# Kernel tuning notes

Measured on AMD Instinct MI355X. Metric: run time of the kernel, lower is better.

## Reference

```python
import jax, jax.numpy as jnp
import numpy as np
from math import factorial, pi, sqrt

N_ATOMS = 4096
N_PAIRS = 49152
F = 16           # num_tensordense_features
NUM_RADIAL = 16  # basis num=16
NUM_SPECIES = 95
EMB_DIM = 32
CUTOFF = 5.0
LMAX = 4         # SelfAttention max_degree=4
NLM = 25
LMAX_B = 2       # basis max_degree=2 (also max_tensordense_degree)
NLM_B = 9

DEG9 = np.repeat(np.arange(3), [1, 3, 5])        # degree index of each lm, l<=2
DEG25 = np.repeat(np.arange(5), [1, 3, 5, 7, 9]) # degree index of each lm, l<=4


def real_sph(u, lmax):
    # real spherical harmonics (m = -l..l ordering, no Condon-Shortley), u: (...,3) unit vectors
    x, y, z = u[..., 0], u[..., 1], u[..., 2]
    phi = jnp.arctan2(y, x)
    ct = jnp.clip(z, -1.0, 1.0)
    st = jnp.sqrt(jnp.clip(1.0 - ct * ct, 0.0, 1.0))
    P = {(0, 0): jnp.ones_like(ct)}
    for m in range(1, lmax + 1):
        P[(m, m)] = -(2 * m - 1) * st * P[(m - 1, m - 1)]
    for m in range(0, lmax):
        P[(m + 1, m)] = (2 * m + 1) * ct * P[(m, m)]
    for m in range(0, lmax + 1):
        for l in range(m + 2, lmax + 1):
            P[(l, m)] = ((2 * l - 1) * ct * P[(l - 1, m)] - (l + m - 1) * P[(l - 2, m)]) / (l - m)
    outs = []
    for l in range(lmax + 1):
        for m in range(-l, l + 1):
            ma = abs(m)
            Nn = sqrt((2 * l + 1) / (4 * pi) * factorial(l - ma) / factorial(l + ma))
            cs = (-1.0) ** ma  # cancel Condon-Shortley in P
            if m == 0:
                Y = Nn * P[(l, 0)]
            elif m > 0:
                Y = sqrt(2.0) * Nn * cs * jnp.cos(m * phi) * P[(l, m)]
            else:
                Y = sqrt(2.0) * Nn * cs * jnp.sin(ma * phi) * P[(l, ma)]
            outs.append(Y)
    return jnp.stack(outs, axis=-1)


def _gaunt():
    # exact real Gaunt (CG-equivalent) coupling coefficients via Gauss-Legendre x uniform-phi quadrature
    nt, nph = 16, 32
    xs, ws = np.polynomial.legendre.leggauss(nt)
    phis = np.arange(nph) * (2 * np.pi / nph)
    ct = np.repeat(xs, nph); ph = np.tile(phis, nt)
    st = np.sqrt(np.clip(1.0 - ct ** 2, 0.0, 1.0))
    u = np.stack([st * np.cos(ph), st * np.sin(ph), ct], -1)
    w = np.repeat(ws, nph) * (2 * np.pi / nph)
    Y = np.asarray(real_sph(jnp.asarray(u, dtype=jnp.float32), LMAX))
    G = np.einsum('gi,gj,gk,g->ijk', Y, Y[:, :NLM_B], Y, w)
    G[np.abs(G) < 1e-6] = 0.0
    return G

_G = _gaunt()
G_ATT = jnp.asarray(_G, dtype=jnp.float32)                      # (25, 9, 25): feat x basis -> feat
G_TD = jnp.asarray(_G[:NLM_B, :, :NLM_B], dtype=jnp.float32)    # (9, 9, 9): TensorDense coupling


def pdense(x, W, deg):
    return jnp.einsum('plf,lfg->plg', x, W[deg])


def couple(xf, Bf, G):
    # equivariant tensor product  out[p,k,f] = sum_ij G[i,j,k] xf[p,i,f] Bf[p,j,f]
    u = jnp.einsum('pif,ijk->pjkf', xf, G)
    return jnp.einsum('pjf,pjkf->pkf', Bf, u)


def setup_inputs() -> dict:
    key = jax.random.key(0)
    ks = jax.random.split(key, 24)
    s = 1.0 / np.sqrt(F)
    inp = dict(
        atomic_numbers=jax.random.randint(ks[0], (N_ATOMS,), 0, NUM_SPECIES),
        neighbour_indices=jnp.stack([
            jax.random.randint(ks[1], (N_PAIRS,), 0, N_ATOMS),
            jax.random.randint(ks[2], (N_PAIRS,), 0, N_ATOMS)], axis=-1),
        neighbour_displacements=jax.random.normal(ks[3], (N_PAIRS, 3), dtype=jnp.float32) * 1.7,
        W_rad=jax.random.normal(ks[4], (NUM_SPECIES, NUM_RADIAL, F), dtype=jnp.float32) / np.sqrt(NUM_RADIAL),
        emb_table=jax.random.normal(ks[5], (NUM_SPECIES, EMB_DIM), dtype=jnp.float32),
        W_emb=jax.random.normal(ks[6], (EMB_DIM, F), dtype=jnp.float32) / np.sqrt(EMB_DIM),
        b_emb=jnp.zeros((F,), jnp.float32),
        td_W1=jax.random.normal(ks[7], (3, F, F), dtype=jnp.float32) * s,
        td_W2=jax.random.normal(ks[8], (3, F, F), dtype=jnp.float32) * s,
        td_W3=jax.random.normal(ks[9], (3, F, F), dtype=jnp.float32) * s,
        Wb1=jax.random.normal(ks[10], (NUM_RADIAL, F), dtype=jnp.float32) / np.sqrt(NUM_RADIAL),
        Wq1=jax.random.normal(ks[11], (5, F, F), dtype=jnp.float32) * s,
        Wk1=jax.random.normal(ks[12], (5, F, F), dtype=jnp.float32) * s,
        Wv1=jax.random.normal(ks[13], (5, F, F), dtype=jnp.float32) * s,
        Wo1=jax.random.normal(ks[14], (5, F, F), dtype=jnp.float32) * s,
        bo1=jnp.zeros((F,), jnp.float32),
        Wb2=jax.random.normal(ks[15], (NUM_RADIAL, F), dtype=jnp.float32) / np.sqrt(NUM_RADIAL),
        Wq2=jax.random.normal(ks[16], (5, F, F), dtype=jnp.float32) * s,
        Wk2=jax.random.normal(ks[17], (5, F, F), dtype=jnp.float32) * s,
        Wv2=jax.random.normal(ks[18], (5, F, F), dtype=jnp.float32) * s,
        Wo2=jax.random.normal(ks[19], (5, F, F), dtype=jnp.float32) * s,
        bo2=jnp.zeros((F,), jnp.float32),
    )
    return inp


def reference(atomic_numbers, neighbour_indices, neighbour_displacements,
              W_rad, emb_table, W_emb, b_emb, td_W1, td_W2, td_W3,
              Wb1, Wq1, Wk1, Wv1, Wo1, bo1, Wb2, Wq2, Wk2, Wv2, Wo2, bo2):
    dst = neighbour_indices[:, 0]   # idx_i
    src = neighbour_indices[:, 1]   # idx_j
    Zj = atomic_numbers[src]
    r = jnp.linalg.norm(neighbour_displacements, axis=-1)
    u = neighbour_displacements / jnp.maximum(r, 1e-9)[:, None]
    sh = real_sph(u, LMAX)          # (P, 25)
    sh_b = sh[:, :NLM_B]            # (P, 9)
    kk = jnp.arange(1, NUM_RADIAL + 1, dtype=jnp.float32)
    rb = jnp.sinc(kk[None, :] * r[:, None] / CUTOFF) * (r < CUTOFF)[:, None]  # sinc basis w/ cutoff
    # species-aware radial basis -> per-pair equivariant features (P, 9, F)
    y0 = jnp.einsum('pk,pkf->pf', rb, W_rad[Zj])
    y = sh_b[:, :, None] * y0[:, None, :]
    # TensorDense: dense -> CG tensor product -> dense (degrees <= 2)
    a = pdense(y, td_W1, DEG9)
    b = pdense(y, td_W2, DEG9)
    u9 = jnp.einsum('pif,ijk->pjkf', a, G_TD)
    tp = jnp.einsum('pjf,pjkf->pkf', b, u9)
    y = pdense(tp, td_W3, DEG9)
    # aggregate per-pair messages to atoms (segment mean), pad degrees to l<=4
    sums = jnp.zeros((N_ATOMS, NLM_B, F), y.dtype).at[dst].add(y)
    cnt = jnp.zeros((N_ATOMS,), y.dtype).at[dst].add(1.0)
    x = sums / jnp.maximum(cnt, 1.0)[:, None, None]
    x = jnp.pad(x, ((0, 0), (0, NLM - NLM_B), (0, 0)))  # (N, 25, F)
    # two segment self-attention layers over neighbour pairs
    for (Wb, Wq, Wk, Wv, Wo, bo) in ((Wb1, Wq1, Wk1, Wv1, Wo1, bo1), (Wb2, Wq2, Wk2, Wv2, Wo2, bo2)):
        Bf = sh_b[:, :, None] * (rb @ Wb)[:, None, :]   # projected pair basis (P, 9, F)
        q = pdense(x, Wq, DEG25)[dst]
        kf = couple(pdense(x, Wk, DEG25)[src], Bf, G_ATT)
        vf = couple(pdense(x, Wv, DEG25)[src], Bf, G_ATT)
        s = jnp.einsum('plf,plf->p', q, kf) / np.sqrt(NLM * F)
        m = jax.lax.stop_gradient(jnp.full((N_ATOMS,), -1e30, s.dtype).at[dst].max(s))
        e = jnp.exp(s - m[dst])
        den = jnp.zeros((N_ATOMS,), s.dtype).at[dst].add(e)
        alpha = e / (den[dst] + 1e-9)
        agg = jnp.zeros((N_ATOMS, NLM, F), x.dtype).at[dst].add(alpha[:, None, None] * vf)
        x = pdense(agg, Wo, DEG25)
        x = x.at[:, 0, :].add(bo)
    # embedding residual connection on the scalar (l=0) channel
    res = emb_table[atomic_numbers] @ W_emb + b_emb
    x = x.at[:, 0, :].add(res)
    return x
```

## Files before the change

### kernel.cpp

```cpp
#include <hip/hip_runtime.h>
#include <hip/hip_bf16.h>

#define NA 4096
#define NP 49152

typedef _Float16 f16;
typedef _Float16 h2 __attribute__((ext_vector_type(2)));
union U4H { uint4 u; f16 h[8]; h2 p[4]; };

__device__ __forceinline__ float fdot2(h2 a, h2 b, float c){
#if __has_builtin(__builtin_amdgcn_fdot2)
  return __builtin_amdgcn_fdot2(a, b, c, false);
#else
  return c + (float)a.x*(float)b.x + (float)a.y*(float)b.y;
#endif
}

constexpr int WS_AOFS9 = 64;
constexpr int WS_ATTW9 = 128;
constexpr int WS_ATTIJ9= WS_ATTW9 + 512;
constexpr int WS_G     = 12800;
constexpr int WS_NATT  = WS_G + 5632;
constexpr int WS_ATTW  = WS_NATT + 8;
constexpr int WS_ATTIJ = WS_ATTW + 1024;
constexpr int WS_TDOFS = WS_ATTIJ + 1024;
constexpr int WS_TDW   = WS_TDOFS + 16;
constexpr int WS_TDIJ  = WS_TDW + 512;
constexpr int WS_AOFS  = WS_TDIJ + 512;
constexpr int WS_SH    = WS_AOFS + 32;
constexpr int WS_RB    = WS_SH + NP*9;
constexpr int WS_S     = WS_RB + NP*16;
constexpr int WS_CCNT  = WS_S + NP;
constexpr int WS_COFF  = WS_CCNT + NA;
constexpr int WS_CCUR  = WS_COFF + NA + 8;
constexpr int WS_CLST  = WS_CCUR + NA;
constexpr int WS_XQ    = WS_CLST + NP;
constexpr int WS_XK    = WS_XQ + NA*400;
constexpr int WS_XV    = WS_XK + NA*400;
constexpr int WS_PVF   = WS_XV + NA*400;
constexpr int WS_WW    = WS_PVF + NP*128;
constexpr int WS_PVFE  = WS_PVF + NP*256;
constexpr int WS_DS    = WS_PVFE;
constexpr long long WS_END = (long long)WS_DS + 2*NP + 16;

__device__ const float  GLX[16] = {
  -0.98940093499164993f, -0.94457502307323258f, -0.86563120238783174f, -0.75540440835500303f,
  -0.61787624440264375f, -0.45801677765722739f, -0.28160355077925891f, -0.09501250983763744f,
   0.09501250983763744f,  0.28160355077925891f,  0.45801677765722739f,  0.61787624440264375f,
   0.75540440835500303f,  0.86563120238783174f,  0.94457502307323258f,  0.98940093499164993f };
__device__ const double GLW[16] = {
  0.02715245941175409, 0.06225352393864789, 0.09515851168249278, 0.12462897125553387,
  0.14959598881657673, 0.16915651939500254, 0.18260341504492359, 0.18945061045506850,
  0.18945061045506850, 0.18260341504492359, 0.16915651939500254, 0.14959598881657673,
  0.12462897125553387, 0.09515851168249278, 0.06225352393864789, 0.02715245941175409 };

#define PI_D 3.14159265358979323846

__device__ __forceinline__ float scrub(float v){
  if(!(v == v)) return 0.f;
  return fminf(fmaxf(v, -1e30f), 1e30f);
}

__device__ void real_sph25(float ct, float phi, float* Y){
  float st = sqrtf(fmaxf(0.f, 1.f - ct*ct));
  float P[5][5];
  P[0][0] = 1.f;
  #pragma unroll
  for(int m=1;m<=4;m++) P[m][m] = -(2.f*m - 1.f)*st*P[m-1][m-1];
  #pragma unroll
  for(int m=0;m<4;m++) P[m+1][m] = (2.f*m + 1.f)*ct*P[m][m];
  #pragma unroll
  for(int m=0;m<=4;m++){
    #pragma unroll
    for(int l=m+2;l<=4;l++)
      P[l][m] = ((2.f*l - 1.f)*ct*P[l-1][m] - (float)(l+m-1)*P[l-2][m]) / (float)(l-m);
  }
  const double fact[9] = {1,1,2,6,24,120,720,5040,40320};
  int idx = 0;
  #pragma unroll
  for(int l=0;l<=4;l++){
    #pragma unroll
    for(int m=-l;m<=l;m++){
      int ma = (m < 0) ? -m : m;
      float Nn = (float)sqrt((2*l+1)/(4.0*PI_D)*fact[l-ma]/fact[l+ma]);
      float cs = (ma & 1) ? -1.f : 1.f;
      float v;
      if(m == 0)      v = Nn * P[l][0];
      else if(m > 0)  v = 1.4142135623730951f * Nn * cs * cosf(ma*phi) * P[l][ma];
      else            v = 1.4142135623730951f * Nn * cs * sinf(ma*phi) * P[l][ma];
      Y[idx++] = v;
    }
  }
}

__global__ __launch_bounds__(256) void k_u1(const float* Wrad, const float* W1,
    const float* W2, const int* nbr, float* ws){
  __shared__ float Ysh[12800];
  int b = blockIdx.x, tid = threadIdx.x;
  if(b < 176){
    for(int pt=tid; pt<512; pt+=256){
      float ct  = GLX[pt >> 5];
      float phi = (float)((pt & 31) * (2.0*PI_D/32.0));
      float Y[25];
      real_sph25(ct, phi, Y);
      #pragma unroll
      for(int i=0;i<25;i++) Ysh[pt*25 + i] = Y[i];
    }
    __syncthreads();
    int idx = b*256 + tid;
    int t = idx >> 3, chunk = idx & 7;
    if(t >= 5625) return;
    int k = t % 25, j = (t/25) % 9, i = t/225;
    double acc = 0.0;
    int g0 = chunk*64;
    #pragma unroll 4
    for(int g=g0; g<g0+64; g++){
      double w = GLW[g >> 5] * (2.0*PI_D/32.0);
      acc += w * (double)Ysh[g*25+i] * (double)Ysh[g*25+j] * (double)Ysh[g*25+k];
    }
    acc += __shfl_xor(acc, 1, 8);
    acc += __shfl_xor(acc, 2, 8);
    acc += __shfl_xor(acc, 4, 8);
    if(chunk == 0){
      if(fabs(acc) < 1e-6) acc = 0.0;
      ws[WS_G + (i*9+j)*25 + k] = (float)acc;
    }
  } else if(b < 271){
    int s = b - 176;
    #pragma unroll
    for(int it=0; it<6; it++){
      int idx = tid + 256*it;
      int w = idx / 768, r = idx % 768;
      int d = r / 256, r2 = r % 256, k = r2 / 16, g = r2 % 16;
      const float* Wsrc = (w == 0) ? W1 : W2;
      float acc = 0.f;
      #pragma unroll
      for(int fp=0; fp<16; fp++)
        acc += Wrad[(s*16+k)*16+fp] * Wsrc[(d*16+fp)*16+g];
      ws[WS_WW + ((size_t)(s*2+w)*16 + g)*48 + d*16 + k] = acc;
    }
  } else {
    int p = (b-271)*256 + tid;
    if(p < NP) atomicAdd((int*)ws + WS_CCNT + nbr[2*p], 1);
  }
}

__global__ __launch_bounds__(1024) void k_scan(float* ws){
  __shared__ int wsum[17];
  int t = threadIdx.x;
  const int* cnt = (const int*)ws + WS_CCNT;
  int v0 = cnt[4*t], v1 = cnt[4*t+1], v2 = cnt[4*t+2], v3 = cnt[4*t+3];
  int s = v0+v1+v2+v3;
  int lane = t & 63, w = t >> 6;
  int x = s;
  #pragma unroll
  for(int o=1;o<64;o<<=1){
    int y = __shfl_up(x, o);
    if(lane >= o) x += y;
  }
  if(lane == 63) wsum[w] = x;
  __syncthreads();
  if(t == 0){
    int run = 0;
    #pragma unroll
    for(int i=0;i<16;i++){ int tmp = wsum[i]; wsum[i] = run; run += tmp; }
    wsum[16] = run;
  }
  __syncthreads();
  int base = wsum[w] + x - s;
  int* offp = (int*)ws + WS_COFF;
  int* cur  = (int*)ws + WS_CCUR;
  offp[4*t]   = base;          cur[4*t]   = base;
  offp[4*t+1] = base+v0;       cur[4*t+1] = base+v0;
  offp[4*t+2] = base+v0+v1;    cur[4*t+2] = base+v0+v1;
  offp[4*t+3] = base+v0+v1+v2; cur[4*t+3] = base+v0+v1+v2;
  if(t == 1023) offp[4096] = wsum[16];
}

__global__ __launch_bounds__(256) void k_u2(const float* disp, const int* nbr, float* ws){
  __shared__ float Gsh[5632];
  __shared__ int cA[25], cT[9], cA9[25], oA[26], oT[10], oA9[26];
  if(blockIdx.x == 0){
    int t = threadIdx.x;
    for(int i=t; i<5625; i+=256) Gsh[i] = ws[WS_G + i];
    __syncthreads();
    const float* G = Gsh;
    if(t < 25){
      int c=0, c9=0;
      for(int i=0;i<25;i++) for(int j=0;j<9;j++) if(G[(i*9+j)*25+t] != 0.f){ c++; if(i<9) c9++; }
      cA[t]=c; cA9[t]=c9;
    }
    if(t < 9){ int c=0; for(int i=0;i<9;i++) for(int j=0;j<9;j++) if(G[(i*9+j)*25+t] != 0.f) c++; cT[t]=c; }
    __syncthreads();
    if(t == 0){
      int s=0; for(int k=0;k<25;k++){ oA[k]=s; s+=cA[k]; } oA[25]=s;
      ((int*)ws)[WS_NATT] = s;
      s=0; for(int k=0;k<25;k++){ oA9[k]=s; s+=cA9[k]; } oA9[25]=s;
      s=0; for(int k=0;k<9;k++){ oT[k]=s; s+=cT[k]; } oT[9]=s;
    }
    __syncthreads();
    float* attw = ws + WS_ATTW;  int* attij = (int*)ws + WS_ATTIJ;
    float* attw9 = ws + WS_ATTW9; int* attij9 = (int*)ws + WS_ATTIJ9;
    int* aofs  = (int*)ws + WS_AOFS;
    int* aofs9 = (int*)ws + WS_AOFS9;
    if(t < 26){ aofs[t] = oA[t] < 1024 ? oA[t] : 1024; aofs9[t] = oA9[t] < 512 ? oA9[t] : 512; }
    if(t < 25){
      int pos = oA[t], pos9 = oA9[t];
      for(int i=0;i<25;i++) for(int j=0;j<9;j++){
        float w = G[(i*9+j)*25+t];
        if(w != 0.f){
          if(pos < 1024){ attw[pos]=w; attij[pos] = i | (j<<5) | (t<<9); pos++; }
          if(i < 9 && pos9 < 512){ attw9[pos9]=w; attij9[pos9] = i | (j<<5) | (t<<9); pos9++; }
        }
      }
    }
    float* tdw = ws + WS_TDW; int* tdij = (int*)ws + WS_TDIJ; int* tdofs = (int*)ws + WS_TDOFS;
    if(t < 9){
      int pos = oT[t];
      for(int i=0;i<9;i++) for(int j=0;j<9;j++){
        float w = G[(i*9+j)*25+t];
        if(w != 0.f && pos < 512){
          int li = (i==0)?0:(i<4)?1:2, lj = (j==0)?0:(j<4)?1:2;
          tdw[pos]=w; tdij[pos] = i | (j<<5) | (li<<10) | (lj<<12); pos++;
        }
      }
      tdofs[t] = oT[t];
      if(t == 0) tdofs[9] = oT[9];
    }
  } else {
    int p = (blockIdx.x-1)*256 + threadIdx.x;
    if(p >= NP) return;
    int d = nbr[2*p], s = nbr[2*p+1];
    int sp = atomicAdd((int*)ws + WS_CCUR + d, 1);
    ((int*)ws)[WS_DS + 2*sp]     = d;
    ((int*)ws)[WS_DS + 2*sp + 1] = s;
    float dx = disp[3*p], dy = disp[3*p+1], dz = disp[3*p+2];
    float r = sqrtf(dx*dx + dy*dy + dz*dz);
    float inv = 1.f / fmaxf(r, 1e-9f);
    float ux = dx*inv, uy = dy*inv, uz = dz*inv;
    float sh[9];
    sh[0] = 0.28209479177387814f;
    sh[1] = 0.4886025119029199f * uy;
    sh[2] = 0.4886025119029199f * uz;
    sh[3] = 0.4886025119029199f * ux;
    sh[4] = 1.0925484305920792f * ux*uy;
    sh[5] = 1.0925484305920792f * uy*uz;
    sh[6] = 0.31539156525252005f * (3.f*uz*uz - 1.f);
    sh[7] = 1.0925484305920792f * ux*uz;
    sh[8] = 0.5462742152960396f * (ux*ux - uy*uy);
    #pragma unroll
    for(int i=0;i<9;i++) ws[WS_SH + sp*9 + i] = scrub(sh[i]);
    float mask = (r < 5.f) ? 1.f : 0.f;
    float rbv[16];
    #pragma unroll
    for(int k=1;k<=16;k++){
      float x  = (float)k * r * 0.2f;
      float px = 3.14159265358979323846f * x;
      float s2 = (px < 1e-6f) ? 1.f : (sinf(px)/px);
      rbv[k-1] = scrub(s2 * mask);
    }
    float4* rb4 = (float4*)(ws + WS_RB + sp*16);
    #pragma unroll
    for(int c=0;c<4;c++) rb4[c] = make_float4(rbv[4*c], rbv[4*c+1], rbv[4*c+2], rbv[4*c+3]);
  }
}

__global__ __launch_bounds__(256) void k_td(const int* aZ, const float* W3, float* ws){
  __shared__ float sh_s[16][9];
  __shared__ float S_s[16][88];
  __shared__ float tp_s[16][9][16];
  int tid = threadIdx.x, pl = tid >> 4, g = tid & 15;
  int sp = blockIdx.x*16 + pl;
  int src = ((const int*)ws)[WS_DS + 2*sp + 1];
  int Zj = aZ[src];
  {
    float4* S4 = (float4*)&S_s[0][0];
    for(int t0=tid; t0<352; t0+=256) S4[t0] = make_float4(0.f,0.f,0.f,0.f);
  }
  if(g < 9) sh_s[pl][g] = ws[WS_SH + sp*9 + g];
  float rb[16];
  {
    const float4* rb4 = (const float4*)(ws + WS_RB + sp*16);
    #pragma unroll
    for(int c=0;c<4;c++){
      float4 r = rb4[c];
      rb[4*c]=r.x; rb[4*c+1]=r.y; rb[4*c+2]=r.z; rb[4*c+3]=r.w;
    }
  }
  float A1[3], A2[3];
  {
    const float4* w1 = (const float4*)(ws + WS_WW + ((size_t)(Zj*2+0)*16+g)*48);
    const float4* w2 = (const float4*)(ws + WS_WW + ((size_t)(Zj*2+1)*16+g)*48);
    #pragma unroll
    for(int d=0; d<3; d++){
      float a1 = 0.f, a2 = 0.f;
      #pragma unroll
      for(int c=0;c<4;c++){
        float4 x1 = w1[d*4+c], x2 = w2[d*4+c];
        a1 += x1.x*rb[4*c] + x1.y*rb[4*c+1] + x1.z*rb[4*c+2] + x1.w*rb[4*c+3];
        a2 += x2.x*rb[4*c] + x2.y*rb[4*c+1] + x2.z*rb[4*c+2] + x2.w*rb[4*c+3];
      }
      A1[d] = a1; A2[d] = a2;
    }
  }
  __syncthreads();
  if(g < 9){
    const float* tdw = ws + WS_TDW;
    const int* tdij  = (const int*)ws + WS_TDIJ;
    const int* tdofs = (const int*)ws + WS_TDOFS;
    int e1 = tdofs[g+1];
    for(int e=tdofs[g]; e<e1; e++){
      float w = tdw[e]; int meta = tdij[e];
      int i = meta & 31, j = (meta>>5) & 15, li = (meta>>10) & 3, lj = (meta>>12) & 3;
      S_s[pl][g*9 + li*3 + lj] += w * sh_s[pl][i] * sh_s[pl][j];
    }
  }
  __syncthreads();
  float AA[9];
  #pragma unroll
  for(int li=0;li<3;li++)
    #pragma unroll
    for(int lj=0;lj<3;lj++) AA[li*3+lj] = A1[li]*A2[lj];
  #pragma unroll
  for(int k=0;k<9;k++){
    float tpv = 0.f;
    #pragma unroll
    for(int c=0;c<9;c++) tpv += S_s[pl][k*9+c] * AA[c];
    tp_s[pl][k][g] = tpv;
  }
  __syncthreads();
  float w3r[48];
  #pragma unroll
  for(int d=0;d<3;d++)
    #pragma unroll
    for(int f2=0;f2<16;f2++) w3r[d*16+f2] = W3[(d*16+f2)*16+g];
  float acc9[9];
  #pragma unroll
  for(int k=0;k<9;k++){
    int d = (k==0)?0:(k<4)?1:2;
    const float4* t4 = (const float4*)&tp_s[pl][k][0];
    float acc = 0.f;
    #pragma unroll
    for(int c=0;c<4;c++){
      float4 t = t4[c];
      acc += t.x*w3r[d*16+4*c] + t.y*w3r[d*16+4*c+1] + t.z*w3r[d*16+4*c+2] + t.w*w3r[d*16+4*c+3];
    }
    acc9[k] = scrub(acc);
  }
  f16* ptd = (f16*)(ws + WS_PVF) + (size_t)sp*256 + g*16;
  U4H u0, u1;
  #pragma unroll
  for(int j=0;j<8;j++) u0.h[j] = (f16)acc9[j];
  u1.h[0] = (f16)acc9[8];
  #pragma unroll
  for(int j=1;j<8;j++) u1.h[j] = (f16)0.f;
  *(uint4*)(ptd)     = u0.u;
  *(uint4*)(ptd + 8) = u1.u;
}

__global__ __launch_bounds__(256) void k_tdq(const float* Wq, const float* Wk,
                                             const float* Wv, float* ws){
  __shared__ float xsh[4][144];
  __shared__ float wq_sh[768], wk_sh[768], wv_sh[768];
  int tid = threadIdx.x, al = tid >> 6, lane = tid & 63;
  int a = blockIdx.x*4 + al;
  for(int t=tid; t<768; t+=256){ wq_sh[t]=Wq[t]; wk_sh[t]=Wk[t]; wv_sh[t]=Wv[t]; }
  const int* coff = (const int*)ws + WS_COFF;
  int off0 = coff[a], n = coff[a+1] - off0;
  const f16* base = (const f16*)(ws + WS_PVF);
  float acc[8] = {0,0,0,0,0,0,0,0};
  if(lane < 32){
    for(int t=0; t<n; t++){
      U4H u; u.u = *(const uint4*)(base + (size_t)(off0+t)*256 + lane*8);
      #pragma unroll
      for(int j=0;j<8;j++) acc[j] += (float)u.h[j];
    }
  }
  float invn = 1.f / fmaxf((float)n, 1.f);
  if(lane < 32){
    int gg = lane >> 1;
    #pragma unroll
    for(int j=0;j<8;j++){
      int k = (lane & 1)*8 + j;
      if(k < 9) xsh[al][k*16 + gg] = scrub(acc[j]*invn);
    }
  }
  __syncthreads();
  int g = lane & 15, q4 = lane >> 4;
  f16* qt = (f16*)(ws + WS_XQ) + (size_t)a*800 + g*32;
  f16* kt = (f16*)(ws + WS_XK) + (size_t)a*800 + g*32;
  f16* vt = (f16*)(ws + WS_XV) + (size_t)a*800 + g*32;
  for(int i=q4; i<16; i+=4){
    if(i < 9){
      int l = (i==0)?0:(i<4)?1:2;
      float q=0.f, k2=0.f, v2=0.f;
      #pragma unroll
      for(int f2=0;f2<16;f2++){
        float xv = xsh[al][i*16+f2];
        q  += xv*wq_sh[(l*16+f2)*16+g];
        k2 += xv*wk_sh[(l*16+f2)*16+g];
        v2 += xv*wv_sh[(l*16+f2)*16+g];
      }
      qt[i] = (f16)q; kt[i] = (f16)k2; vt[i] = (f16)v2;
    } else {
      qt[i] = (f16)0.f; kt[i] = (f16)0.f; vt[i] = (f16)0.f;
    }
  }
}

template<int NI>
__global__ __launch_bounds__(128) void k_att(const float* Wb, float* ws){
  constexpr int MROWH = (NI == 9) ? 16 : 32;
  constexpr int PLSTR = (NI == 9) ? 408 : 840;
  __shared__ __align__(16) f16 Ml[8][PLSTR];
  __shared__ float sh_s[8][9];
  __shared__ float wb_sh[256];
  constexpr int NPAIR = NI/2;
  constexpr int TAIL  = NI-1;
  int tid = threadIdx.x, pl = tid >> 4, g = tid & 15;
  int sp = blockIdx.x*8 + pl;
  {
    uint4 z; z.x=0; z.y=0; z.z=0; z.w=0;
    uint4* Mz = (uint4*)&Ml[0][0];
    for(int t0=tid; t0<PLSTR; t0+=128) Mz[t0] = z;
  }
  for(int t0=tid; t0<256; t0+=128) wb_sh[t0] = Wb[t0];
  if(g < 9) sh_s[pl][g] = ws[WS_SH + sp*9 + g];
  __syncthreads();
  {
    const float* attw = ws + (NI==9 ? WS_ATTW9 : WS_ATTW);
    const int* attij  = (const int*)ws + (NI==9 ? WS_ATTIJ9 : WS_ATTIJ);
    const int* aofs   = (const int*)ws + (NI==9 ? WS_AOFS9 : WS_AOFS);
    for(int kr=g; kr<25; kr+=16){
      f16* Mrow = &Ml[pl][kr*MROWH];
      int e = aofs[kr], e1 = aofs[kr+1];
      if(e < e1){
        int meta = attij[e];
        int curi = meta & 31;
        float cur = 0.f;
        for(; e<e1; e++){
          meta = attij[e];
          int i2 = meta & 31;
          if(i2 != curi){ Mrow[curi] = (f16)cur; cur = 0.f; curi = i2; }
          cur += attw[e] * sh_s[pl][(meta>>5) & 15];
        }
        Mrow[curi] = (f16)cur;
      }
    }
  }
  __syncthreads();
  int dst = ((const int*)ws)[WS_DS + 2*sp];
  int src = ((const int*)ws)[WS_DS + 2*sp + 1];
  float q_r[NI];
  {
    const f16* qt = (const f16*)(ws + WS_XQ) + (size_t)dst*800 + g*32;
    #pragma unroll
    for(int c=0;c<NPAIR/4;c++){
      U4H u; u.u = *(const uint4*)(qt + c*8);
      #pragma unroll
      for(int j=0;j<8;j++) q_r[c*8+j] = (float)u.h[j];
    }
    q_r[TAIL] = (float)qt[TAIL];
  }
  h2 xk2[NPAIR], xv2[NPAIR];
  float xkT, xvT;
  {
    const f16* kt = (const f16*)(ws + WS_XK) + (size_t)src*800 + g*32;
    const f16* vt = (const f16*)(ws + WS_XV) + (size_t)src*800 + g*32;
    #pragma unroll
    for(int c=0;c<NPAIR/4;c++){
      U4H uk; uk.u = *(const uint4*)(kt + c*8);
      U4H uv; uv.u = *(const uint4*)(vt + c*8);
      #pragma unroll
      for(int j=0;j<4;j++){ xk2[c*4+j] = uk.p[j]; xv2[c*4+j] = uv.p[j]; }
    }
    xkT = (float)kt[TAIL];
    xvT = (float)vt[TAIL];
  }
  float wbf;
  {
    const float4* rb4 = (const float4*)(ws + WS_RB + sp*16);
    float acc = 0.f;
    #pragma unroll
    for(int c=0;c<4;c++){
      float4 r = rb4[c];
      acc += r.x*wb_sh[(4*c)*16+g] + r.y*wb_sh[(4*c+1)*16+g]
           + r.z*wb_sh[(4*c+2)*16+g] + r.w*wb_sh[(4*c+3)*16+g];
    }
    wbf = acc;
  }
  f16* pvf = (f16*)(ws + WS_PVF) + (size_t)sp*400;
  float sacc = 0.f;
  #pragma unroll
  for(int k=0;k<25;k++){
    const uint4* Mq = (const uint4*)&Ml[pl][k*MROWH];
    float mT = (float)Ml[pl][k*MROWH + TAIL];
    float vv = 0.f, kf = 0.f;
    #pragma unroll
    for(int c=0;c<NPAIR/4;c++){
      U4H u; u.u = Mq[c];
      #pragma unroll
      for(int j=0;j<4;j++){
        vv = fdot2(u.p[j], xv2[c*4+j], vv);
        if(k < NI) kf = fdot2(u.p[j], xk2[c*4+j], kf);
      }
    }
    vv += mT * xvT;
    if(k < NI){
      kf += mT * xkT;
      sacc += q_r[k]*kf;
    }
    pvf[k*16 + g] = (f16)scrub(wbf*vv);
  }
  float sl = sacc;
  #pragma unroll
  for(int off=1; off<16; off<<=1) sl += __shfl_xor(sl, off, 16);
  if(g == 0) ws[WS_S + sp] = scrub(sl * 0.05f);
}

template<bool FINAL>
__global__ __launch_bounds__(256) void k_aggo(const float* Wo, const float* bo,
    const int* aZ, const float* emb, const float* Wemb, const float* bemb,
    const float* Wq, const float* Wk, const float* Wv, float* ws, float* out){
  __shared__ float xsh[4][400];
  __shared__ float esh[4][64];
  __shared__ float wo_sh[1280];
  __shared__ float wq_sh[FINAL?4:1280], wk_sh[FINAL?4:1280], wv_sh[FINAL?4:1280];
  __shared__ float osh[FINAL?4:1600];
  int tid = threadIdx.x, al = tid >> 6, lane = tid & 63;
  int a = blockIdx.x*4 + al;
  for(int t=tid; t<1280; t+=256){
    wo_sh[t] = Wo[t];
    if(!FINAL){ wq_sh[t]=Wq[t]; wk_sh[t]=Wk[t]; wv_sh[t]=Wv[t]; }
  }
  const int* coff = (const int*)ws + WS_COFF;
  int off0 = coff[a], n = coff[a+1] - off0;
  float mx = -1e30f;
  for(int t=lane; t<n; t+=64) mx = fmaxf(mx, ws[WS_S + off0 + t]);
  #pragma unroll
  for(int off=1; off<64; off<<=1) mx = fmaxf(mx, __shfl_xor(mx, off));
  float den = 0.f;
  for(int t=lane; t<n; t+=64){
    float e = expf(fminf(ws[WS_S + off0 + t] - mx, 0.f));
    if(t < 64) esh[al][t] = e;
    den += e;
  }
  #pragma unroll
  for(int off=1; off<64; off<<=1) den += __shfl_xor(den, off);
  float inv_den = 1.f / (den + 1e-9f);
  __syncthreads();
  float acc[8] = {0,0,0,0,0,0,0,0}, acc2[8] = {0,0,0,0,0,0,0,0};
  const f16* base = (const f16*)(ws + WS_PVF);
  int t = 0;
  for(; t+1 < n; t += 2){
    float a0 = (t   < 64 ? esh[al][t]   : expf(fminf(ws[WS_S+off0+t  ]-mx,0.f))) * inv_den;
    float a1 = (t+1 < 64 ? esh[al][t+1] : expf(fminf(ws[WS_S+off0+t+1]-mx,0.f))) * inv_den;
    if(lane < 50){
      U4H u0; u0.u = *(const uint4*)(base + (size_t)(off0+t  )*400 + lane*8);
      U4H u1; u1.u = *(const uint4*)(base + (size_t)(off0+t+1)*400 + lane*8);
      #pragma unroll
      for(int j=0;j<8;j++){ acc[j] += a0*(float)u0.h[j]; acc2[j] += a1*(float)u1.h[j]; }
    }
  }
  if(t < n){
    float a0 = (t < 64 ? esh[al][t] : expf(fminf(ws[WS_S+off0+t]-mx,0.f))) * inv_den;
    if(lane < 50){
      U4H u0; u0.u = *(const uint4*)(base + (size_t)(off0+t)*400 + lane*8);
      #pragma unroll
      for(int j=0;j<8;j++) acc[j] += a0*(float)u0.h[j];
    }
  }
  if(lane < 50){
    #pragma unroll
    for(int j=0;j<8;j++) xsh[al][lane*8 + j] = scrub(acc[j] + acc2[j]);
  }
  __syncthreads();
  int g = lane & 15, q4 = lane >> 4;
  for(int i=q4; i<25; i+=4){
    int l = (i==0)?0:(i<4)?1:(i<9)?2:(i<16)?3:4;
    float accv = 0.f;
    #pragma unroll
    for(int f2=0;f2<16;f2++) accv += xsh[al][i*16+f2]*wo_sh[(l*16+f2)*16+g];
    if(i == 0){
      accv += bo[g];
      if(FINAL){
        int Z = aZ[a];
        float res = bemb[g];
        #pragma unroll
        for(int e2=0;e2<32;e2++) res += emb[Z*32+e2]*Wemb[e2*16+g];
        accv += res;
      }
    }
    if(FINAL) out[a*400 + i*16 + g] = scrub(accv);
    else      osh[al*400 + i*16 + g] = scrub(accv);
  }
  if(!FINAL){
    __syncthreads();
    f16* qt = (f16*)(ws + WS_XQ) + (size_t)a*800 + g*32;
    f16* kt = (f16*)(ws + WS_XK) + (size_t)a*800 + g*32;
    f16* vt = (f16*)(ws + WS_XV) + (size_t)a*800 + g*32;
    for(int i=q4; i<25; i+=4){
      int l = (i==0)?0:(i<4)?1:(i<9)?2:(i<16)?3:4;
      float q=0.f, k2=0.f, v2=0.f;
      #pragma unroll
      for(int f2=0;f2<16;f2++){
        float xv = osh[al*400 + i*16 + f2];
        q  += xv*wq_sh[(l*16+f2)*16+g];
        k2 += xv*wk_sh[(l*16+f2)*16+g];
        v2 += xv*wv_sh[(l*16+f2)*16+g];
      }
      qt[i] = (f16)q; kt[i] = (f16)k2; vt[i] = (f16)v2;
    }
  }
}

extern "C" void kernel_launch(void* const* d_in, const int* in_sizes, int n_in,
                              void* d_out, int out_size, void* d_ws, size_t ws_size,
                              hipStream_t stream){
  (void)in_sizes; (void)n_in; (void)out_size;
  if(ws_size < (size_t)WS_END * sizeof(float)) return;
  float* ws = (float*)d_ws;
  const int* aZ  = (const int*)d_in[0];
  const int* nbr = (const int*)d_in[1];
  const float* disp = (const float*)d_in[2];
  const float* Wrad = (const float*)d_in[3];
  const float* emb  = (const float*)d_in[4];
  const float* Wemb = (const float*)d_in[5];
  const float* bemb = (const float*)d_in[6];
  const float* W1   = (const float*)d_in[7];
  const float* W2   = (const float*)d_in[8];
  const float* W3   = (const float*)d_in[9];
  const float* Wb1 = (const float*)d_in[10]; const float* Wq1 = (const float*)d_in[11];
  const float* Wk1 = (const float*)d_in[12]; const float* Wv1 = (const float*)d_in[13];
  const float* Wo1 = (const float*)d_in[14]; const float* bo1 = (const float*)d_in[15];
  const float* Wb2 = (const float*)d_in[16]; const float* Wq2 = (const float*)d_in[17];
  const float* Wk2 = (const float*)d_in[18]; const float* Wv2 = (const float*)d_in[19];
  const float* Wo2 = (const float*)d_in[20]; const float* bo2 = (const float*)d_in[21];

  hipMemsetAsync(ws + WS_CCNT, 0, NA*sizeof(int), stream);
  k_u1<<<463,256,0,stream>>>(Wrad, W1, W2, nbr, ws);
  k_scan<<<1,1024,0,stream>>>(ws);
  k_u2<<<193,256,0,stream>>>(disp, nbr, ws);
  k_td<<<3072,256,0,stream>>>(aZ, W3, ws);
  k_tdq<<<1024,256,0,stream>>>(Wq1, Wk1, Wv1, ws);

  k_att<9><<<6144,128,0,stream>>>(Wb1, ws);
  k_aggo<false><<<1024,256,0,stream>>>(Wo1, bo1, aZ, emb, Wemb, bemb,
                                       Wq2, Wk2, Wv2, ws, nullptr);
  k_att<25><<<6144,128,0,stream>>>(Wb2, ws);
  k_aggo<true><<<1024,256,0,stream>>>(Wo2, bo2, aZ, emb, Wemb, bemb,
                                      nullptr, nullptr, nullptr, ws, (float*)d_out);
}
```

Before: 375.1 us.

## Compute per-pair attention coupling with MFMA 16x16x32 f16 instead of fdot2 loops

The per-pair coupling of K/V features with the Gaunt-weighted basis matrix moves from scalar fdot2 loops to matrix-core MFMA 16x16x32 f16 instructions. Each wave of 64 lanes now handles one pair, with the matrix padded to 32 rows, and the grid doubles to four pairs per 256-thread block. The projected q/k/v feature arrays are zero-padded out to 32 entries so the MFMA operands read clean zeros. This targets the ALU-bound inner dot-product loop. In exchange it adds padded work and a full-wave shuffle reduction, and the intra-block sync after building M is dropped, which relies on each wave writing and reading only its own matrix.

```diff
diff --git a/kernel.cpp b/kernel.cpp
--- a/kernel.cpp
+++ b/kernel.cpp
@@ -6,15 +6,9 @@
 
 typedef _Float16 f16;
 typedef _Float16 h2 __attribute__((ext_vector_type(2)));
-union U4H { uint4 u; f16 h[8]; h2 p[4]; };
-
-__device__ __forceinline__ float fdot2(h2 a, h2 b, float c){
-#if __has_builtin(__builtin_amdgcn_fdot2)
-  return __builtin_amdgcn_fdot2(a, b, c, false);
-#else
-  return c + (float)a.x*(float)b.x + (float)a.y*(float)b.y;
-#endif
-}
+typedef _Float16 f16x8 __attribute__((ext_vector_type(8)));
+typedef float f32x4 __attribute__((ext_vector_type(4)));
+union U4H { uint4 u; f16 h[8]; h2 p[4]; f16x8 v; };
 
 constexpr int WS_AOFS9 = 64;
 constexpr int WS_ATTW9 = 128;
@@ -390,7 +384,7 @@
   f16* qt = (f16*)(ws + WS_XQ) + (size_t)a*800 + g*32;
   f16* kt = (f16*)(ws + WS_XK) + (size_t)a*800 + g*32;
   f16* vt = (f16*)(ws + WS_XV) + (size_t)a*800 + g*32;
-  for(int i=q4; i<16; i+=4){
+  for(int i=q4; i<32; i+=4){
     if(i < 9){
       int l = (i==0)?0:(i<4)?1:2;
       float q=0.f, k2=0.f, v2=0.f;
@@ -409,74 +403,58 @@
 }
 
 template<int NI>
-__global__ __launch_bounds__(128) void k_att(const float* Wb, float* ws){
-  constexpr int MROWH = (NI == 9) ? 16 : 32;
-  constexpr int PLSTR = (NI == 9) ? 408 : 840;
-  __shared__ __align__(16) f16 Ml[8][PLSTR];
-  __shared__ float sh_s[8][9];
+__global__ __launch_bounds__(256) void k_att(const float* Wb, float* ws){
+  constexpr int MROWH = 40;
+  __shared__ __align__(16) f16 Ml[4][32*MROWH];
+  __shared__ float sh_s[4][12];
   __shared__ float wb_sh[256];
-  constexpr int NPAIR = NI/2;
-  constexpr int TAIL  = NI-1;
-  int tid = threadIdx.x, pl = tid >> 4, g = tid & 15;
-  int sp = blockIdx.x*8 + pl;
+  int tid = threadIdx.x;
+  int w = tid >> 6, l = tid & 63;
+  int g = l & 15, quad = l >> 4;
+  int sp = blockIdx.x*4 + w;
   {
     uint4 z; z.x=0; z.y=0; z.z=0; z.w=0;
-    uint4* Mz = (uint4*)&Ml[0][0];
-    for(int t0=tid; t0<PLSTR; t0+=128) Mz[t0] = z;
-  }
-  for(int t0=tid; t0<256; t0+=128) wb_sh[t0] = Wb[t0];
-  if(g < 9) sh_s[pl][g] = ws[WS_SH + sp*9 + g];
-  __syncthreads();
-  {
+    uint4* Mz = (uint4*)&Ml[w][0];
+    for(int t=l; t<32*MROWH/8; t+=64) Mz[t] = z;
+  }
+  if(l < 9) sh_s[w][l] = ws[WS_SH + sp*9 + l];
+  for(int t=tid; t<256; t+=256) wb_sh[t] = Wb[t];
+  __syncthreads();
+  if(l < 25){
     const float* attw = ws + (NI==9 ? WS_ATTW9 : WS_ATTW);
     const int* attij  = (const int*)ws + (NI==9 ? WS_ATTIJ9 : WS_ATTIJ);
     const int* aofs   = (const int*)ws + (NI==9 ? WS_AOFS9 : WS_AOFS);
-    for(int kr=g; kr<25; kr+=16){
-      f16* Mrow = &Ml[pl][kr*MROWH];
-      int e = aofs[kr], e1 = aofs[kr+1];
-      if(e < e1){
-        int meta = attij[e];
-        int curi = meta & 31;
-        float cur = 0.f;
-        for(; e<e1; e++){
-          meta = attij[e];
-          int i2 = meta & 31;
-          if(i2 != curi){ Mrow[curi] = (f16)cur; cur = 0.f; curi = i2; }
-          cur += attw[e] * sh_s[pl][(meta>>5) & 15];
-        }
-        Mrow[curi] = (f16)cur;
+    f16* Mrow = &Ml[w][l*MROWH];
+    int e = aofs[l], e1 = aofs[l+1];
+    if(e < e1){
+      int meta = attij[e];
+      int curi = meta & 31;
+      float cur = 0.f;
+      for(; e<e1; e++){
+        meta = attij[e];
+        int i2 = meta & 31;
+        if(i2 != curi){ Mrow[curi] = (f16)cur; cur = 0.f; curi = i2; }
+        cur += attw[e] * sh_s[w][(meta>>5) & 15];
       }
-    }
-  }
-  __syncthreads();
+      Mrow[curi] = (f16)cur;
+    }
+  }
   int dst = ((const int*)ws)[WS_DS + 2*sp];
   int src = ((const int*)ws)[WS_DS + 2*sp + 1];
-  float q_r[NI];
-  {
-    const f16* qt = (const f16*)(ws + WS_XQ) + (size_t)dst*800 + g*32;
-    #pragma unroll
-    for(int c=0;c<NPAIR/4;c++){
-      U4H u; u.u = *(const uint4*)(qt + c*8);
-      #pragma unroll
-      for(int j=0;j<8;j++) q_r[c*8+j] = (float)u.h[j];
-    }
-    q_r[TAIL] = (float)qt[TAIL];
-  }
-  h2 xk2[NPAIR], xv2[NPAIR];
-  float xkT, xvT;
-  {
-    const f16* kt = (const f16*)(ws + WS_XK) + (size_t)src*800 + g*32;
-    const f16* vt = (const f16*)(ws + WS_XV) + (size_t)src*800 + g*32;
-    #pragma unroll
-    for(int c=0;c<NPAIR/4;c++){
-      U4H uk; uk.u = *(const uint4*)(kt + c*8);
-      U4H uv; uv.u = *(const uint4*)(vt + c*8);
-      #pragma unroll
-      for(int j=0;j<4;j++){ xk2[c*4+j] = uk.p[j]; xv2[c*4+j] = uv.p[j]; }
-    }
-    xkT = (float)kt[TAIL];
-    xvT = (float)vt[TAIL];
-  }
+  U4H ubv, ubk;
+  ubv.u = *(const uint4*)((const f16*)(ws + WS_XV) + (size_t)src*800 + g*32 + quad*8);
+  ubk.u = *(const uint4*)((const f16*)(ws + WS_XK) + (size_t)src*800 + g*32 + quad*8);
+  f16x8 a1 = *(const f16x8*)&Ml[w][(l & 15)*MROWH + quad*8];
+  f16x8 a2 = *(const f16x8*)&Ml[w][(16 + (l & 15))*MROWH + quad*8];
+  f32x4 cv  = {0.f,0.f,0.f,0.f};
+  f32x4 cv2 = {0.f,0.f,0.f,0.f};
+  f32x4 ck  = {0.f,0.f,0.f,0.f};
+  f32x4 ck2 = {0.f,0.f,0.f,0.f};
+  cv  = __builtin_amdgcn_mfma_f32_16x16x32_f16(a1, ubv.v, cv,  0, 0, 0);
+  cv2 = __builtin_amdgcn_mfma_f32_16x16x32_f16(a2, ubv.v, cv2, 0, 0, 0);
+  ck  = __builtin_amdgcn_mfma_f32_16x16x32_f16(a1, ubk.v, ck,  0, 0, 0);
+  if(NI == 25)
+    ck2 = __builtin_amdgcn_mfma_f32_16x16x32_f16(a2, ubk.v, ck2, 0, 0, 0);
   float wbf;
   {
     const float4* rb4 = (const float4*)(ws + WS_RB + sp*16);
@@ -490,32 +468,20 @@
     wbf = acc;
   }
   f16* pvf = (f16*)(ws + WS_PVF) + (size_t)sp*400;
+  const f16* qt = (const f16*)(ws + WS_XQ) + (size_t)dst*800 + g*32;
   float sacc = 0.f;
   #pragma unroll
-  for(int k=0;k<25;k++){
-    const uint4* Mq = (const uint4*)&Ml[pl][k*MROWH];
-    float mT = (float)Ml[pl][k*MROWH + TAIL];
-    float vv = 0.f, kf = 0.f;
-    #pragma unroll
-    for(int c=0;c<NPAIR/4;c++){
-      U4H u; u.u = Mq[c];
-      #pragma unroll
-      for(int j=0;j<4;j++){
-        vv = fdot2(u.p[j], xv2[c*4+j], vv);
-        if(k < NI) kf = fdot2(u.p[j], xk2[c*4+j], kf);
-      }
-    }
-    vv += mT * xvT;
-    if(k < NI){
-      kf += mT * xkT;
-      sacc += q_r[k]*kf;
-    }
-    pvf[k*16 + g] = (f16)scrub(wbf*vv);
-  }
-  float sl = sacc;
-  #pragma unroll
-  for(int off=1; off<16; off<<=1) sl += __shfl_xor(sl, off, 16);
-  if(g == 0) ws[WS_S + sp] = scrub(sl * 0.05f);
+  for(int r=0;r<4;r++){
+    int k  = quad*4 + r;
+    int k2 = 16 + k;
+    pvf[k*16 + g] = (f16)scrub(wbf*cv[r]);
+    if(k2 < 25) pvf[k2*16 + g] = (f16)scrub(wbf*cv2[r]);
+    sacc += (float)qt[k] * ck[r];
+    if(NI == 25) sacc += (float)qt[k2] * ck2[r];
+  }
+  #pragma unroll
+  for(int off=1; off<64; off<<=1) sacc += __shfl_xor(sacc, off);
+  if(l == 0) ws[WS_S + sp] = scrub(sacc * 0.05f);
 }
 
 template<bool FINAL>
@@ -599,17 +565,21 @@
     f16* qt = (f16*)(ws + WS_XQ) + (size_t)a*800 + g*32;
     f16* kt = (f16*)(ws + WS_XK) + (size_t)a*800 + g*32;
     f16* vt = (f16*)(ws + WS_XV) + (size_t)a*800 + g*32;
-    for(int i=q4; i<25; i+=4){
-      int l = (i==0)?0:(i<4)?1:(i<9)?2:(i<16)?3:4;
-      float q=0.f, k2=0.f, v2=0.f;
-      #pragma unroll
-      for(int f2=0;f2<16;f2++){
-        float xv = osh[al*400 + i*16 + f2];
-        q  += xv*wq_sh[(l*16+f2)*16+g];
-        k2 += xv*wk_sh[(l*16+f2)*16+g];
-        v2 += xv*wv_sh[(l*16+f2)*16+g];
+    for(int i=q4; i<32; i+=4){
+      if(i < 25){
+        int l = (i==0)?0:(i<4)?1:(i<9)?2:(i<16)?3:4;
+        float q=0.f, k2=0.f, v2=0.f;
+        #pragma unroll
+        for(int f2=0;f2<16;f2++){
+          float xv = osh[al*400 + i*16 + f2];
+          q  += xv*wq_sh[(l*16+f2)*16+g];
+          k2 += xv*wk_sh[(l*16+f2)*16+g];
+          v2 += xv*wv_sh[(l*16+f2)*16+g];
+        }
+        qt[i] = (f16)q; kt[i] = (f16)k2; vt[i] = (f16)v2;
+      } else {
+        qt[i] = (f16)0.f; kt[i] = (f16)0.f; vt[i] = (f16)0.f;
       }
-      qt[i] = (f16)q; kt[i] = (f16)k2; vt[i] = (f16)v2;
     }
   }
 }
@@ -644,10 +614,10 @@
   k_td<<<3072,256,0,stream>>>(aZ, W3, ws);
   k_tdq<<<1024,256,0,stream>>>(Wq1, Wk1, Wv1, ws);
 
-  k_att<9><<<6144,128,0,stream>>>(Wb1, ws);
+  k_att<9><<<12288,256,0,stream>>>(Wb1, ws);
   k_aggo<false><<<1024,256,0,stream>>>(Wo1, bo1, aZ, emb, Wemb, bemb,
                                        Wq2, Wk2, Wv2, ws, nullptr);
-  k_att<25><<<6144,128,0,stream>>>(Wb2, ws);
+  k_att<25><<<12288,256,0,stream>>>(Wb2, ws);
   k_aggo<true><<<1024,256,0,stream>>>(Wo2, bo2, aZ, emb, Wemb, bemb,
                                       nullptr, nullptr, nullptr, ws, (float*)d_out);
 }
```

Result: slower. 469.1 us (+25.0%).
